# Optimization experiments

Measured on AMD Instinct MI355X. Metric: run time of the kernel, lower is better.

Reference implementation:

```python
import jax, jax.numpy as jnp
import numpy as np

HEADS = 24
HEAD_DIM = 128
DIM = HEADS * HEAD_DIM  # 3072
EPS = 1e-5


def _rms_norm(x, w):
    # x: [B,S,H,D], w: [D]
    var = jnp.mean(jnp.square(x), axis=-1, keepdims=True)
    return x * jax.lax.rsqrt(var + EPS) * w


def _apply_rope(x, cos, sin):
    # non-neox (interleaved pairs): x: [B,S,H,D], cos/sin: [S,D]
    B, S, H, D = x.shape
    xr = x.reshape(B, S, H, D // 2, 2)
    x_real, x_imag = xr[..., 0], xr[..., 1]
    rotated = jnp.stack([-x_imag, x_real], axis=-1).reshape(B, S, H, D)
    c = cos[None, :, None, :]
    s = sin[None, :, None, :]
    return x * c + rotated * s


def setup_inputs() -> dict:
    key = jax.random.key(0)
    ks = jax.random.split(key, 20)
    B, S_img, S_txt = 1, 2048, 512
    S = S_img + S_txt
    sc = 1.0 / np.sqrt(DIM)
    inp = {
        "x": jax.random.normal(ks[0], (B, S_img, DIM), jnp.float32),
        "encoder_hidden_states": jax.random.normal(ks[1], (B, S_txt, DIM), jnp.float32),
        "rope_cos": jax.random.uniform(ks[2], (S, HEAD_DIM), jnp.float32),
        "rope_sin": jax.random.uniform(ks[3], (S, HEAD_DIM), jnp.float32),
        # image-stream projections (bias=False)
        "wq": jax.random.normal(ks[4], (DIM, DIM), jnp.float32) * sc,
        "wk": jax.random.normal(ks[5], (DIM, DIM), jnp.float32) * sc,
        "wv": jax.random.normal(ks[6], (DIM, DIM), jnp.float32) * sc,
        # text-stream projections (added_proj_bias=True)
        "w_add_q": jax.random.normal(ks[7], (DIM, DIM), jnp.float32) * sc,
        "w_add_k": jax.random.normal(ks[8], (DIM, DIM), jnp.float32) * sc,
        "w_add_v": jax.random.normal(ks[9], (DIM, DIM), jnp.float32) * sc,
        "b_add_q": jax.random.normal(ks[10], (DIM,), jnp.float32) * 0.01,
        "b_add_k": jax.random.normal(ks[11], (DIM,), jnp.float32) * 0.01,
        "b_add_v": jax.random.normal(ks[12], (DIM,), jnp.float32) * 0.01,
        # per-head RMSNorm weights
        "norm_q_w": jnp.ones((HEAD_DIM,), jnp.float32),
        "norm_k_w": jnp.ones((HEAD_DIM,), jnp.float32),
        "norm_aq_w": jnp.ones((HEAD_DIM,), jnp.float32),
        "norm_ak_w": jnp.ones((HEAD_DIM,), jnp.float32),
        # output projections (out_bias=True)
        "w_out": jax.random.normal(ks[13], (DIM, DIM), jnp.float32) * sc,
        "b_out": jax.random.normal(ks[14], (DIM,), jnp.float32) * 0.01,
        "w_add_out": jax.random.normal(ks[15], (DIM, DIM), jnp.float32) * sc,
        "b_add_out": jax.random.normal(ks[16], (DIM,), jnp.float32) * 0.01,
    }
    return inp


def reference(x, encoder_hidden_states, rope_cos, rope_sin,
              wq, wk, wv, w_add_q, w_add_k, w_add_v,
              b_add_q, b_add_k, b_add_v,
              norm_q_w, norm_k_w, norm_aq_w, norm_ak_w,
              w_out, b_out, w_add_out, b_add_out):
    B, S_img, _ = x.shape
    S_txt = encoder_hidden_states.shape[1]

    def proj(h, w, b=None):
        y = jnp.einsum('bsd,ed->bse', h, w)
        return y if b is None else y + b

    def heads(t):
        return t.reshape(B, t.shape[1], HEADS, HEAD_DIM)

    q = _rms_norm(heads(proj(x, wq)), norm_q_w)
    k = _rms_norm(heads(proj(x, wk)), norm_k_w)
    v = heads(proj(x, wv))

    eq = _rms_norm(heads(proj(encoder_hidden_states, w_add_q, b_add_q)), norm_aq_w)
    ek = _rms_norm(heads(proj(encoder_hidden_states, w_add_k, b_add_k)), norm_ak_w)
    ev = heads(proj(encoder_hidden_states, w_add_v, b_add_v))

    # encoder tokens first, then image tokens
    q = jnp.concatenate([eq, q], axis=1)
    k = jnp.concatenate([ek, k], axis=1)
    v = jnp.concatenate([ev, v], axis=1)

    q = _apply_rope(q, rope_cos, rope_sin)
    k = _apply_rope(k, rope_cos, rope_sin)

    scale = 1.0 / np.sqrt(HEAD_DIM)
    scores = jnp.einsum('bqhd,bkhd->bhqk', q, k) * scale
    attn = jax.nn.softmax(scores, axis=-1)
    o = jnp.einsum('bhqk,bkhd->bqhd', attn, v)
    o = o.reshape(B, S_txt + S_img, DIM)

    enc_o, img_o = o[:, :S_txt], o[:, S_txt:]
    img_out = jnp.einsum('bsd,ed->bse', img_o, w_out) + b_out
    enc_out = jnp.einsum('bsd,ed->bse', enc_o, w_add_out) + b_add_out
    return img_out, enc_out
```

## Files before the change

### kernel.cpp

```cpp
#include <hip/hip_runtime.h>
#include <hip/hip_bf16.h>


typedef __hip_bfloat16 bf16;
typedef __attribute__((ext_vector_type(8))) short short8;
typedef __attribute__((ext_vector_type(4))) short s16x4;
typedef __attribute__((ext_vector_type(4))) float f32x4;

#define KDIM 3072
#define S_TXT 512
#define S_IMG 2048
#define S_ALL 2560
#define NHEADS 24
#define HDIM 128
#define WELEM (KDIM * KDIM)
#define AELEM (S_ALL * KDIM)
#define NSPLIT 3
#define NT_K 48
#define QBN 192

__device__ __forceinline__ void async_ld16(const void* g, void* l) {
  __builtin_amdgcn_global_load_lds((__attribute__((address_space(1))) void*)g,
                                   (__attribute__((address_space(3))) void*)l,
                                   16, 0, 0);
}

__device__ __forceinline__ short bf16_bits(float x) {
  bf16 h = (bf16)x;
  return __builtin_bit_cast(short, h);
}
__device__ __forceinline__ float bits_f32(short s) {
  return (float)__builtin_bit_cast(bf16, s);
}

__global__ __launch_bounds__(256) void cast_weights_kernel(
    const float* __restrict__ w0, const float* __restrict__ w1,
    const float* __restrict__ w2, const float* __restrict__ w3,
    const float* __restrict__ w4, const float* __restrict__ w5,
    const float* __restrict__ w6, const float* __restrict__ w7,
    bf16* __restrict__ dst) {
  const float* srcs[8] = {w0, w1, w2, w3, w4, w5, w6, w7};
  const float* __restrict__ src = srcs[blockIdx.y];
  bf16* __restrict__ out = dst + (size_t)blockIdx.y * WELEM;
  const size_t i0 = ((size_t)blockIdx.x * 256 + threadIdx.x) * 8;
  const float4 f0 = *(const float4*)(src + i0);
  const float4 f1 = *(const float4*)(src + i0 + 4);
  short8 o;
  o[0] = bf16_bits(f0.x); o[1] = bf16_bits(f0.y);
  o[2] = bf16_bits(f0.z); o[3] = bf16_bits(f0.w);
  o[4] = bf16_bits(f1.x); o[5] = bf16_bits(f1.y);
  o[6] = bf16_bits(f1.z); o[7] = bf16_bits(f1.w);
  *(short8*)(out + i0) = o;
}

__global__ __launch_bounds__(256) void cast_acts_kernel(
    const float* __restrict__ x, const float* __restrict__ enc,
    bf16* __restrict__ xe) {
  const size_t i0 = ((size_t)blockIdx.x * 256 + threadIdx.x) * 8;
  const size_t TXT = (size_t)S_TXT * KDIM;
  const float* __restrict__ src = (i0 < TXT) ? (enc + i0) : (x + (i0 - TXT));
  const float4 f0 = *(const float4*)(src);
  const float4 f1 = *(const float4*)(src + 4);
  short8 o;
  o[0] = bf16_bits(f0.x); o[1] = bf16_bits(f0.y);
  o[2] = bf16_bits(f0.z); o[3] = bf16_bits(f0.w);
  o[4] = bf16_bits(f1.x); o[5] = bf16_bits(f1.y);
  o[6] = bf16_bits(f1.z); o[7] = bf16_bits(f1.w);
  *(short8*)(xe + i0) = o;
}

template <typename OutT, bool TRANS>
__device__ __forceinline__ void gemm256(const bf16* __restrict__ Ab,
                                        const bf16* __restrict__ Bb,
                                        OutT* __restrict__ C,
                                        const float* __restrict__ bias,
                                        short* sAmem, short* sBmem) {
  const int tid = threadIdx.x;
  const int lane = tid & 63;
  const int w = tid >> 6;
  const int a = lane & 15;
  const int g = (lane >> 4) & 3;
  const int wm = w >> 1;
  const int wn = w & 1;

  short* const A0h0 = sAmem;
  short* const A0h1 = sAmem + 8192;
  short* const A1h0 = sAmem + 16384;
  short* const A1h1 = sAmem + 24576;
  short* const B0h0 = sBmem;
  short* const B0h1 = sBmem + 6144;
  short* const B1h0 = sBmem + 12288;
  short* const B1h1 = sBmem + 18432;

  auto stageA = [&](int kbase, short* lblk) {
#pragma unroll
    for (int l = 0; l < 2; l++) {
      const int t = l * 512 + tid;
      const int row = t >> 2;
      const int ls = (t & 3) ^ ((row >> 1) & 3);
      async_ld16(Ab + (size_t)row * KDIM + kbase + ls * 8,
                 lblk + (l * 512 + w * 64) * 8);
    }
  };
  auto stageB = [&](int kbase, short* lblk) {
    {
      const int t = tid;
      const int row = t >> 2;
      const int ls = (t & 3) ^ ((row >> 1) & 3);
      async_ld16(Bb + (size_t)row * KDIM + kbase + ls * 8,
                 lblk + (w * 64) * 8);
    }
    if (w < 4) {
      const int t = 512 + tid;
      const int row = t >> 2;
      const int ls = (t & 3) ^ ((row >> 1) & 3);
      async_ld16(Bb + (size_t)row * KDIM + kbase + ls * 8,
                 lblk + (512 + w * 64) * 8);
    }
  };
  auto frag = [&](const short* lblk, int R) -> short8 {
    return *(const short8*)(lblk + R * 32 + ((g ^ ((R >> 1) & 3)) * 8));
  };

  f32x4 acc[4][6] = {};

  stageA(0, A0h0);
  stageA(32, A0h1);
  stageB(0, B0h0);
  stageB(32, B0h1);
  asm volatile("s_waitcnt vmcnt(0)" ::: "memory");
  __builtin_amdgcn_s_barrier();

  const int ra = wm * 64 + a;
  const int rb = wn * 96 + a;

  auto ktile = [&](int u, const short* cA0, const short* cA1,
                   const short* cB0, const short* cB1,
                   short* nA0, short* nA1, short* nB0, short* nB1) {
    short8 af0[4], af1[4], b0a[3], b0b[3], b1a[3], b1b[3];
#pragma unroll
    for (int i = 0; i < 4; i++) af0[i] = frag(cA0, ra + i * 16);
#pragma unroll
    for (int j = 0; j < 3; j++) b0a[j] = frag(cB0, rb + j * 16);
    __builtin_amdgcn_sched_barrier(0);
#pragma unroll
    for (int j = 0; j < 3; j++) b0b[j] = frag(cB0, rb + (j + 3) * 16);
    __builtin_amdgcn_sched_barrier(0);
#pragma unroll
    for (int i = 0; i < 4; i++) af1[i] = frag(cA1, ra + i * 16);
#pragma unroll
    for (int j = 0; j < 3; j++) b1a[j] = frag(cB1, rb + j * 16);
    __builtin_amdgcn_sched_barrier(0);
#pragma unroll
    for (int j = 0; j < 3; j++) b1b[j] = frag(cB1, rb + (j + 3) * 16);
    __builtin_amdgcn_sched_barrier(0);
    if (u + 1 < NT_K) {
      const int kb = (u + 1) * 64;
      stageA(kb, nA0);
      stageA(kb + 32, nA1);
      stageB(kb, nB0);
      stageB(kb + 32, nB1);
    }
    __builtin_amdgcn_sched_barrier(0);
    asm volatile("s_waitcnt lgkmcnt(13)" ::: "memory");
    __builtin_amdgcn_sched_barrier(0);
    __builtin_amdgcn_s_setprio(1);
#pragma unroll
    for (int i = 0; i < 4; i++)
#pragma unroll
      for (int j = 0; j < 3; j++)
        acc[i][j] = __builtin_amdgcn_mfma_f32_16x16x32_bf16(af0[i], b0a[j], acc[i][j], 0, 0, 0);
    __builtin_amdgcn_s_setprio(0);
    __builtin_amdgcn_sched_barrier(0);
    asm volatile("s_waitcnt lgkmcnt(10)" ::: "memory");
    __builtin_amdgcn_sched_barrier(0);
    __builtin_amdgcn_s_setprio(1);
#pragma unroll
    for (int i = 0; i < 4; i++)
#pragma unroll
      for (int j = 0; j < 3; j++)
        acc[i][j + 3] = __builtin_amdgcn_mfma_f32_16x16x32_bf16(af0[i], b0b[j], acc[i][j + 3], 0, 0, 0);
    __builtin_amdgcn_s_setprio(0);
    __builtin_amdgcn_sched_barrier(0);
    asm volatile("s_waitcnt lgkmcnt(3)" ::: "memory");
    __builtin_amdgcn_sched_barrier(0);
    __builtin_amdgcn_s_setprio(1);
#pragma unroll
    for (int i = 0; i < 4; i++)
#pragma unroll
      for (int j = 0; j < 3; j++)
        acc[i][j] = __builtin_amdgcn_mfma_f32_16x16x32_bf16(af1[i], b1a[j], acc[i][j], 0, 0, 0);
    __builtin_amdgcn_s_setprio(0);
    __builtin_amdgcn_sched_barrier(0);
    asm volatile("s_waitcnt lgkmcnt(0)" ::: "memory");
    __builtin_amdgcn_sched_barrier(0);
    __builtin_amdgcn_s_setprio(1);
#pragma unroll
    for (int i = 0; i < 4; i++)
#pragma unroll
      for (int j = 0; j < 3; j++)
        acc[i][j + 3] = __builtin_amdgcn_mfma_f32_16x16x32_bf16(af1[i], b1b[j], acc[i][j + 3], 0, 0, 0);
    __builtin_amdgcn_s_setprio(0);
    __builtin_amdgcn_sched_barrier(0);
    asm volatile("s_waitcnt vmcnt(0)" ::: "memory");
    __builtin_amdgcn_s_barrier();
  };

#pragma unroll 1
  for (int u = 0; u < NT_K; u += 2) {
    ktile(u,     A0h0, A0h1, B0h0, B0h1, A1h0, A1h1, B1h0, B1h1);
    ktile(u + 1, A1h0, A1h1, B1h0, B1h1, A0h0, A0h1, B0h0, B0h1);
  }

  if constexpr (TRANS) {
#pragma unroll
    for (int i = 0; i < 4; i++)
#pragma unroll
      for (int j = 0; j < 6; j++) {
        const int col = wn * 96 + j * 16 + a;
        const float bv = bias ? bias[col] : 0.0f;
        s16x4 pk;
#pragma unroll
        for (int r = 0; r < 4; r++) pk[r] = bf16_bits(acc[i][j][r] + bv);
        *(s16x4*)((short*)C + (size_t)col * S_ALL + wm * 64 + i * 16 + g * 4) = pk;
      }
  } else {
#pragma unroll
    for (int i = 0; i < 4; i++)
#pragma unroll
      for (int j = 0; j < 6; j++) {
        const int col = wn * 96 + j * 16 + a;
        const float bv = bias ? bias[col] : 0.0f;
#pragma unroll
        for (int r = 0; r < 4; r++) {
          const int row = wm * 64 + i * 16 + g * 4 + r;
          C[(size_t)row * KDIM + col] = (OutT)(acc[i][j][r] + bv);
        }
      }
  }
}

__global__ __launch_bounds__(512, 2) void qkv_kernel(
    const bf16* __restrict__ XE, const bf16* __restrict__ Wc,
    const float* __restrict__ bq, const float* __restrict__ bk, const float* __restrict__ bv,
    bf16* __restrict__ Q, bf16* __restrict__ K, bf16* __restrict__ VT) {
  __shared__ alignas(16) short sAmem[4 * 8192];
  __shared__ alignas(16) short sBmem[4 * 6144];
  const int bid = blockIdx.x;
  const int wk_ = (bid & 7) * 60 + (bid >> 3);
  const int bm = wk_ / 48;
  const int bn = wk_ % 48;
  const int which = bn / 16;
  const int nc = (bn % 16) * QBN;
  const bool txt = bm < 2;
  const bf16* W = Wc + (size_t)(txt ? (3 + which) : which) * WELEM + (size_t)nc * KDIM;
  const float* bias = nullptr;
  if (txt) bias = ((which == 0) ? bq : (which == 1) ? bk : bv) + nc;
  const int crow = bm * 256;
  const bf16* A = XE + (size_t)crow * KDIM;
  if (which == 2) {
    gemm256<bf16, true>(A, W, VT + (size_t)nc * S_ALL + crow, bias, sAmem, sBmem);
  } else {
    bf16* Out = (which == 0) ? Q : K;
    gemm256<bf16, false>(A, W, Out + (size_t)crow * KDIM + nc, bias, sAmem, sBmem);
  }
}

template <typename OutT, bool TRANS>
__device__ __forceinline__ void gemm_tile(const bf16* __restrict__ A,
                                          const bf16* __restrict__ B,
                                          OutT* __restrict__ C,
                                          const float* __restrict__ bias) {
  __shared__ alignas(16) short sA[128 * 32];
  __shared__ alignas(16) short sB[128 * 32];
  const int tid = threadIdx.x;
  const int lane = tid & 63;
  const int w = tid >> 6;
  const int a = lane & 15;
  const int g = lane >> 4;
  const int wm = (w >> 1) * 64;
  const int wn = (w & 1) * 64;

  f32x4 acc[4][4] = {};

  const int s0 = tid, s1 = tid + 256;
  const int r0 = s0 >> 2, b0 = (s0 & 3) ^ ((r0 >> 1) & 3);
  const int r1 = s1 >> 2, b1 = (s1 & 3) ^ ((r1 >> 1) & 3);
  const bf16* gA0 = A + (size_t)r0 * KDIM + b0 * 8;
  const bf16* gA1 = A + (size_t)r1 * KDIM + b1 * 8;
  const bf16* gB0 = B + (size_t)r0 * KDIM + b0 * 8;
  const bf16* gB1 = B + (size_t)r1 * KDIM + b1 * 8;
  short* lA0 = sA + (w * 64) * 8;
  short* lA1 = sA + (256 + w * 64) * 8;
  short* lB0 = sB + (w * 64) * 8;
  short* lB1 = sB + (256 + w * 64) * 8;

  for (int k0 = 0; k0 < KDIM; k0 += 32) {
    __syncthreads();
    async_ld16(gA0 + k0, lA0);
    async_ld16(gA1 + k0, lA1);
    async_ld16(gB0 + k0, lB0);
    async_ld16(gB1 + k0, lB1);
    __syncthreads();
    short8 af[4], bfg[4];
#pragma unroll
    for (int i = 0; i < 4; i++) {
      const int R = wm + i * 16 + a;
      af[i] = *(const short8*)(sA + R * 32 + ((g ^ ((R >> 1) & 3)) * 8));
    }
#pragma unroll
    for (int j = 0; j < 4; j++) {
      const int R = wn + j * 16 + a;
      bfg[j] = *(const short8*)(sB + R * 32 + ((g ^ ((R >> 1) & 3)) * 8));
    }
#pragma unroll
    for (int i = 0; i < 4; i++)
#pragma unroll
      for (int j = 0; j < 4; j++)
        acc[i][j] = __builtin_amdgcn_mfma_f32_16x16x32_bf16(af[i], bfg[j], acc[i][j], 0, 0, 0);
  }

  if constexpr (TRANS) {
#pragma unroll
    for (int i = 0; i < 4; i++)
#pragma unroll
      for (int j = 0; j < 4; j++) {
        const int col = wn + j * 16 + a;
        const float bv = bias ? bias[col] : 0.0f;
        s16x4 pk;
#pragma unroll
        for (int r = 0; r < 4; r++) pk[r] = bf16_bits(acc[i][j][r] + bv);
        *(s16x4*)((short*)C + (size_t)col * S_ALL + wm + i * 16 + g * 4) = pk;
      }
  } else {
#pragma unroll
    for (int i = 0; i < 4; i++)
#pragma unroll
      for (int j = 0; j < 4; j++) {
        const int col = wn + j * 16 + a;
        const float bv = bias ? bias[col] : 0.0f;
#pragma unroll
        for (int r = 0; r < 4; r++) {
          const int row = wm + i * 16 + g * 4 + r;
          C[(size_t)row * KDIM + col] = (OutT)(acc[i][j][r] + bv);
        }
      }
  }
}

__global__ __launch_bounds__(256) void outproj_kernel(
    const bf16* __restrict__ Obuf, const bf16* __restrict__ Wc,
    const float* __restrict__ b_out, const float* __restrict__ b_add,
    float* __restrict__ out) {
  const int bm = blockIdx.x;
  const int bn = blockIdx.y;
  const bool txt = bm < 4;
  const bf16* A = Obuf + (size_t)bm * 128 * KDIM;
  const bf16* W = Wc + (size_t)(txt ? 7 : 6) * WELEM;
  const float* bias = txt ? b_add : b_out;
  float* C = txt ? (out + (size_t)S_IMG * KDIM + (size_t)bm * 128 * KDIM)
                 : (out + (size_t)(bm - 4) * 128 * KDIM);
  gemm_tile<float, false>(A, W + (size_t)bn * 128 * KDIM, C + bn * 128, bias + bn * 128);
}

__global__ __launch_bounds__(256) void norm_rope_kernel(
    bf16* __restrict__ Q, bf16* __restrict__ K,
    const float* __restrict__ rc, const float* __restrict__ rs,
    const float* __restrict__ nqw, const float* __restrict__ nkw,
    const float* __restrict__ naqw, const float* __restrict__ nakw) {
  const int row = blockIdx.x;
  const int h = blockIdx.y * 4 + (threadIdx.x >> 6);
  const int t = threadIdx.x & 63;
  const long base = (long)row * KDIM + h * HDIM;
  const int d0 = 2 * t, d1 = d0 + 1;
  const bool txt = row < S_TXT;
  const float QSCL = 0.08838834764831845f * 1.4426950408889634f;
  float qa = (float)Q[base + d0], qb = (float)Q[base + d1];
  float ka = (float)K[base + d0], kb = (float)K[base + d1];
  float sq = qa * qa + qb * qb;
  float sk = ka * ka + kb * kb;
#pragma unroll
  for (int m = 1; m < 64; m <<= 1) {
    sq += __shfl_xor(sq, m);
    sk += __shfl_xor(sk, m);
  }
  const float rq = rsqrtf(sq * (1.0f / 128.0f) + 1e-5f) * QSCL;
  const float rk = rsqrtf(sk * (1.0f / 128.0f) + 1e-5f);
  const float* qw = txt ? naqw : nqw;
  const float* kw = txt ? nakw : nkw;
  const float c0 = rc[row * HDIM + d0], c1 = rc[row * HDIM + d1];
  const float s0 = rs[row * HDIM + d0], s1 = rs[row * HDIM + d1];
  const float qn0 = qa * rq * qw[d0], qn1 = qb * rq * qw[d1];
  const float kn0 = ka * rk * kw[d0], kn1 = kb * rk * kw[d1];
  Q[base + d0] = (bf16)(qn0 * c0 - qn1 * s0);
  Q[base + d1] = (bf16)(qn1 * c1 + qn0 * s1);
  K[base + d0] = (bf16)(kn0 * c0 - kn1 * s0);
  K[base + d1] = (bf16)(kn1 * c1 + kn0 * s1);
}

__global__ __launch_bounds__(256) void flash_kernel(
    const bf16* __restrict__ Q, const bf16* __restrict__ Kb,
    const bf16* __restrict__ VT,
    bf16* __restrict__ Op0, bf16* __restrict__ Op1, bf16* __restrict__ Op2,
    float* __restrict__ L) {
  __shared__ alignas(16) short sK[64 * 128];
  __shared__ alignas(16) short sVT[128 * 64];
  __shared__ alignas(16) short sP[4][32 * 72];
  const int tid = threadIdx.x;
  const int lane = tid & 63;
  const int w = tid >> 6;
  const int a = lane & 15;
  const int g = lane >> 4;
  const int qt = blockIdx.x;
  const int h = blockIdx.y;
  const int split = blockIdx.z;
  const int it0 = split * 13;
  const int it1 = (split == 2) ? 40 : (it0 + 13);
  const int qrow0 = qt * 128 + w * 32;
  short* const sPw = sP[w];

  short8 qf[2][4];
#pragma unroll
  for (int mi = 0; mi < 2; mi++)
#pragma unroll
    for (int kk = 0; kk < 4; kk++)
      qf[mi][kk] = *(const short8*)(Q + (size_t)(qrow0 + mi * 16 + a) * KDIM + h * HDIM + kk * 32 + g * 8);

  f32x4 oacc[2][8] = {};
  float lsum[2] = {0.0f, 0.0f};

  for (int it = it0; it < it1; ++it) {
    const int kv0 = it * 64;
    __syncthreads();
#pragma unroll
    for (int is = 0; is < 4; is++) {
      const int s = is * 256 + w * 64 + lane;
      const int kr = s >> 4, p = s & 15;
      const int lb = (p - (kr & 7)) & 15;
      async_ld16(Kb + (size_t)(kv0 + kr) * KDIM + h * HDIM + lb * 8,
                 sK + (is * 256 + w * 64) * 8);
    }
#pragma unroll
    for (int is = 0; is < 4; is++) {
      const int s = is * 256 + w * 64 + lane;
      const int dr = s >> 3, p = s & 7;
      const int lb = (p - (dr & 7)) & 7;
      async_ld16(VT + (size_t)(h * HDIM + dr) * S_ALL + kv0 + lb * 8,
                 sVT + (is * 256 + w * 64) * 8);
    }
    __syncthreads();

    f32x4 st[4][2] = {};
#pragma unroll
    for (int kk = 0; kk < 4; kk++) {
      short8 kf[4];
#pragma unroll
      for (int ni = 0; ni < 4; ni++) {
        const int kr = ni * 16 + a;
        const int p = ((kk * 4 + g) + (kr & 7)) & 15;
        kf[ni] = *(const short8*)(sK + kr * 128 + p * 8);
      }
#pragma unroll
      for (int ni = 0; ni < 4; ni++)
#pragma unroll
        for (int mi = 0; mi < 2; mi++)
          st[ni][mi] = __builtin_amdgcn_mfma_f32_16x16x32_bf16(kf[ni], qf[mi][kk], st[ni][mi], 0, 0, 0);
    }

#pragma unroll
    for (int mi = 0; mi < 2; mi++)
#pragma unroll
      for (int ni = 0; ni < 4; ni++) {
        s16x4 pk;
#pragma unroll
        for (int r = 0; r < 4; r++) {
          const float p = exp2f(st[ni][mi][r]);
          lsum[mi] += p;
          pk[r] = bf16_bits(p);
        }
        *(s16x4*)(sPw + (mi * 16 + a) * 72 + ni * 16 + g * 4) = pk;
      }

#pragma unroll
    for (int ks = 0; ks < 2; ks++) {
      short8 pf[2];
#pragma unroll
      for (int mi = 0; mi < 2; mi++)
        pf[mi] = *(const short8*)(sPw + (mi * 16 + a) * 72 + ks * 32 + g * 8);
#pragma unroll
      for (int nd = 0; nd < 8; nd++) {
        const int dr = nd * 16 + a;
        const int p = ((ks * 4 + g) + (dr & 7)) & 7;
        const short8 vf = *(const short8*)(sVT + dr * 64 + p * 8);
#pragma unroll
        for (int mi = 0; mi < 2; mi++)
          oacc[mi][nd] = __builtin_amdgcn_mfma_f32_16x16x32_bf16(pf[mi], vf, oacc[mi][nd], 0, 0, 0);
      }
    }
  }

#pragma unroll
  for (int mi = 0; mi < 2; mi++) {
    lsum[mi] += __shfl_xor(lsum[mi], 16);
    lsum[mi] += __shfl_xor(lsum[mi], 32);
  }
  bf16* __restrict__ Op = (split == 0) ? Op0 : (split == 1) ? Op1 : Op2;
#pragma unroll
  for (int mi = 0; mi < 2; mi++) {
#pragma unroll
    for (int r = 0; r < 4; r++) {
      const float inv = 1.0f / __shfl(lsum[mi], g * 4 + r);
      const size_t row = qrow0 + mi * 16 + g * 4 + r;
#pragma unroll
      for (int nd = 0; nd < 8; nd++)
        Op[row * KDIM + h * HDIM + nd * 16 + a] = (bf16)(oacc[mi][nd][r] * inv);
    }
    if (g == 0)
      L[((size_t)split * NHEADS + h) * S_ALL + qrow0 + mi * 16 + a] = lsum[mi];
  }
}

__global__ __launch_bounds__(256) void merge_kernel(
    bf16* __restrict__ O0, const bf16* __restrict__ O1, const bf16* __restrict__ O2,
    const float* __restrict__ L) {
  const size_t i0 = ((size_t)blockIdx.x * 256 + threadIdx.x) * 8;
  const int row = (int)(i0 / KDIM);
  const int h = (int)((i0 % KDIM) >> 7);
  const float l0 = L[((size_t)0 * NHEADS + h) * S_ALL + row];
  const float l1 = L[((size_t)1 * NHEADS + h) * S_ALL + row];
  const float l2 = L[((size_t)2 * NHEADS + h) * S_ALL + row];
  const float inv = 1.0f / (l0 + l1 + l2);
  const float w0 = l0 * inv, w1 = l1 * inv, w2 = l2 * inv;
  const short8 v0 = *(const short8*)(O0 + i0);
  const short8 v1 = *(const short8*)(O1 + i0);
  const short8 v2 = *(const short8*)(O2 + i0);
  short8 o;
#pragma unroll
  for (int u = 0; u < 8; u++)
    o[u] = bf16_bits(w0 * bits_f32(v0[u]) + w1 * bits_f32(v1[u]) + w2 * bits_f32(v2[u]));
  *(short8*)(O0 + i0) = o;
}

extern "C" void kernel_launch(void* const* d_in, const int* in_sizes, int n_in,
                              void* d_out, int out_size, void* d_ws, size_t ws_size,
                              hipStream_t stream) {
  const float* x    = (const float*)d_in[0];
  const float* enc  = (const float*)d_in[1];
  const float* rc   = (const float*)d_in[2];
  const float* rs   = (const float*)d_in[3];
  const float* wq   = (const float*)d_in[4];
  const float* wk   = (const float*)d_in[5];
  const float* wv   = (const float*)d_in[6];
  const float* waq  = (const float*)d_in[7];
  const float* wak  = (const float*)d_in[8];
  const float* wav  = (const float*)d_in[9];
  const float* bq   = (const float*)d_in[10];
  const float* bk   = (const float*)d_in[11];
  const float* bv   = (const float*)d_in[12];
  const float* nqw  = (const float*)d_in[13];
  const float* nkw  = (const float*)d_in[14];
  const float* naqw = (const float*)d_in[15];
  const float* nakw = (const float*)d_in[16];
  const float* w_out     = (const float*)d_in[17];
  const float* b_out     = (const float*)d_in[18];
  const float* w_add_out = (const float*)d_in[19];
  const float* b_add_out = (const float*)d_in[20];

  bf16* Wc   = (bf16*)d_ws;
  bf16* XE   = Wc + (size_t)8 * WELEM;
  bf16* Q    = XE + AELEM;
  bf16* K    = Q + AELEM;
  bf16* VT   = K + AELEM;
  bf16* Obuf = VT + AELEM;
  bf16* Op1  = Obuf + AELEM;
  bf16* Op2  = XE;
  float* L   = (float*)(Op1 + AELEM);

  cast_weights_kernel<<<dim3(WELEM / 2048, 8), 256, 0, stream>>>(
      wq, wk, wv, waq, wak, wav, w_out, w_add_out, Wc);
  cast_acts_kernel<<<dim3(AELEM / 2048), 256, 0, stream>>>(x, enc, XE);

  qkv_kernel<<<dim3(480), dim3(512), 0, stream>>>(XE, Wc, bq, bk, bv, Q, K, VT);
  norm_rope_kernel<<<dim3(S_ALL, 6), 256, 0, stream>>>(Q, K, rc, rs, nqw, nkw, naqw, nakw);
  flash_kernel<<<dim3(20, NHEADS, NSPLIT), 256, 0, stream>>>(Q, K, VT, Obuf, Op1, Op2, L);
  merge_kernel<<<dim3(AELEM / 2048), 256, 0, stream>>>(Obuf, Op1, Op2, L);
  outproj_kernel<<<dim3(20, NHEADS), 256, 0, stream>>>(Obuf, Wc, b_out, b_add_out,
                                                       (float*)d_out);
}
```

Baseline: 736.8 us.

## Fuse cast kernels and remap QKV and flash blocks to XCDs for L2 reuse

The weight and activation cast kernels are merged into one launch with an extra grid row for the activations, which removes a launch. The QKV GEMM block mapping is transposed so that blocks on the same XCD share weight column tiles rather than activation rows. The flash kernel moves to a 1D grid that puts all q-tiles and splits of three heads on one XCD, so K/V for a head stays in that XCD's L2, and it adds an occupancy hint of 3 blocks per CU. These remappings change L2 locality, and the occupancy hint may cause register spills.

```diff
diff --git a/kernel.cpp b/kernel.cpp
--- a/kernel.cpp
+++ b/kernel.cpp
@@ -33,32 +33,26 @@
   return (float)__builtin_bit_cast(bf16, s);
 }
 
-__global__ __launch_bounds__(256) void cast_weights_kernel(
+__global__ __launch_bounds__(256) void cast_all_kernel(
     const float* __restrict__ w0, const float* __restrict__ w1,
     const float* __restrict__ w2, const float* __restrict__ w3,
     const float* __restrict__ w4, const float* __restrict__ w5,
     const float* __restrict__ w6, const float* __restrict__ w7,
-    bf16* __restrict__ dst) {
-  const float* srcs[8] = {w0, w1, w2, w3, w4, w5, w6, w7};
-  const float* __restrict__ src = srcs[blockIdx.y];
-  bf16* __restrict__ out = dst + (size_t)blockIdx.y * WELEM;
+    const float* __restrict__ x, const float* __restrict__ enc,
+    bf16* __restrict__ dst, bf16* __restrict__ xe) {
   const size_t i0 = ((size_t)blockIdx.x * 256 + threadIdx.x) * 8;
-  const float4 f0 = *(const float4*)(src + i0);
-  const float4 f1 = *(const float4*)(src + i0 + 4);
-  short8 o;
-  o[0] = bf16_bits(f0.x); o[1] = bf16_bits(f0.y);
-  o[2] = bf16_bits(f0.z); o[3] = bf16_bits(f0.w);
-  o[4] = bf16_bits(f1.x); o[5] = bf16_bits(f1.y);
-  o[6] = bf16_bits(f1.z); o[7] = bf16_bits(f1.w);
-  *(short8*)(out + i0) = o;
-}
-
-__global__ __launch_bounds__(256) void cast_acts_kernel(
-    const float* __restrict__ x, const float* __restrict__ enc,
-    bf16* __restrict__ xe) {
-  const size_t i0 = ((size_t)blockIdx.x * 256 + threadIdx.x) * 8;
-  const size_t TXT = (size_t)S_TXT * KDIM;
-  const float* __restrict__ src = (i0 < TXT) ? (enc + i0) : (x + (i0 - TXT));
+  const float* __restrict__ src;
+  bf16* __restrict__ out;
+  if (blockIdx.y == 8) {
+    if (i0 >= (size_t)AELEM) return;
+    const size_t TXT = (size_t)S_TXT * KDIM;
+    src = (i0 < TXT) ? (enc + i0) : (x + (i0 - TXT));
+    out = xe + i0;
+  } else {
+    const float* srcs[8] = {w0, w1, w2, w3, w4, w5, w6, w7};
+    src = srcs[blockIdx.y] + i0;
+    out = dst + (size_t)blockIdx.y * WELEM + i0;
+  }
   const float4 f0 = *(const float4*)(src);
   const float4 f1 = *(const float4*)(src + 4);
   short8 o;
@@ -66,7 +60,7 @@
   o[2] = bf16_bits(f0.z); o[3] = bf16_bits(f0.w);
   o[4] = bf16_bits(f1.x); o[5] = bf16_bits(f1.y);
   o[6] = bf16_bits(f1.z); o[7] = bf16_bits(f1.w);
-  *(short8*)(xe + i0) = o;
+  *(short8*)(out) = o;
 }
 
 template <typename OutT, bool TRANS>
@@ -248,8 +242,8 @@
   __shared__ alignas(16) short sBmem[4 * 6144];
   const int bid = blockIdx.x;
   const int wk_ = (bid & 7) * 60 + (bid >> 3);
-  const int bm = wk_ / 48;
-  const int bn = wk_ % 48;
+  const int bm = wk_ % 10;
+  const int bn = wk_ / 10;
   const int which = bn / 16;
   const int nc = (bn % 16) * QBN;
   const bool txt = bm < 2;
@@ -398,7 +392,7 @@
   K[base + d1] = (bf16)(kn1 * c1 + kn0 * s1);
 }
 
-__global__ __launch_bounds__(256) void flash_kernel(
+__global__ __launch_bounds__(256, 3) void flash_kernel(
     const bf16* __restrict__ Q, const bf16* __restrict__ Kb,
     const bf16* __restrict__ VT,
     bf16* __restrict__ Op0, bf16* __restrict__ Op1, bf16* __restrict__ Op2,
@@ -411,9 +405,12 @@
   const int w = tid >> 6;
   const int a = lane & 15;
   const int g = lane >> 4;
-  const int qt = blockIdx.x;
-  const int h = blockIdx.y;
-  const int split = blockIdx.z;
+  const int bid = blockIdx.x;
+  const int xcd = bid & 7;
+  const int idx = bid >> 3;
+  const int h = xcd * 3 + idx / 60;
+  const int split = (idx / 20) % 3;
+  const int qt = idx % 20;
   const int it0 = split * 13;
   const int it1 = (split == 2) ? 40 : (it0 + 13);
   const int qrow0 = qt * 128 + w * 32;
@@ -576,13 +573,12 @@
   bf16* Op2  = XE;
   float* L   = (float*)(Op1 + AELEM);
 
-  cast_weights_kernel<<<dim3(WELEM / 2048, 8), 256, 0, stream>>>(
-      wq, wk, wv, waq, wak, wav, w_out, w_add_out, Wc);
-  cast_acts_kernel<<<dim3(AELEM / 2048), 256, 0, stream>>>(x, enc, XE);
+  cast_all_kernel<<<dim3(WELEM / 2048, 9), 256, 0, stream>>>(
+      wq, wk, wv, waq, wak, wav, w_out, w_add_out, x, enc, Wc, XE);
 
   qkv_kernel<<<dim3(480), dim3(512), 0, stream>>>(XE, Wc, bq, bk, bv, Q, K, VT);
   norm_rope_kernel<<<dim3(S_ALL, 6), 256, 0, stream>>>(Q, K, rc, rs, nqw, nkw, naqw, nakw);
-  flash_kernel<<<dim3(20, NHEADS, NSPLIT), 256, 0, stream>>>(Q, K, VT, Obuf, Op1, Op2, L);
+  flash_kernel<<<dim3(1440), 256, 0, stream>>>(Q, K, VT, Obuf, Op1, Op2, L);
   merge_kernel<<<dim3(AELEM / 2048), 256, 0, stream>>>(Obuf, Op1, Op2, L);
   outproj_kernel<<<dim3(20, NHEADS), 256, 0, stream>>>(Obuf, Wc, b_out, b_add_out,
                                                        (float*)d_out);
```

New measurement: 757.0 us. +2.7%, slower.
